# Kernel optimization log

Hardware: AMD Instinct MI355X
Metric: run time of the kernel (lower is better)

## Reference

```python
import jax, jax.numpy as jnp
import numpy as np

# Model dims
B, S, H = 1, 1024, 2048
NH, NKV, DH = 32, 8, 64
G = NH // NKV            # GQA group size
E, K, I = 8, 2, 2048     # experts, top_k, intermediate
ALPHA, LIMIT = 1.702, 7.0
EPS = 1e-5
SCALE = DH ** -0.5


def rmsnorm(x, g):
    return x * jax.lax.rsqrt(jnp.mean(x * x, axis=-1, keepdims=True) + EPS) * g


def setup_inputs() -> dict:
    key = jax.random.key(0)
    ks = jax.random.split(key, 24)
    w = lambda k, shp: jax.random.normal(k, shp, dtype=jnp.float32) * 0.02
    causal = jnp.where(jnp.tril(jnp.ones((S, S), dtype=bool)), 0.0, -1e9).astype(jnp.float32)
    return {
        "hidden_states": jax.random.normal(ks[0], (B, S, H), dtype=jnp.float32),
        "attention_bias": causal[None, None, :, :],           # [1,1,S,S]
        "ln1_g": jnp.ones((H,), jnp.float32),
        "ln2_g": jnp.ones((H,), jnp.float32),
        "Wq": w(ks[1], (NH * DH, H)),  "bq": w(ks[2], (NH * DH,)),
        "Wk": w(ks[3], (NKV * DH, H)), "bk": w(ks[4], (NKV * DH,)),
        "Wv": w(ks[5], (NKV * DH, H)), "bv": w(ks[6], (NKV * DH,)),
        "Wo": w(ks[7], (H, NH * DH)),  "bo": w(ks[8], (H,)),
        "sinks": w(ks[9], (NH,)),
        "router_w": w(ks[10], (E, H)), "router_b": w(ks[11], (E,)),
        "We_gate": w(ks[12], (E, I, H)), "be_gate": w(ks[13], (E, I)),
        "We_up":   w(ks[14], (E, I, H)), "be_up":   w(ks[15], (E, I)),
        "We_down": w(ks[16], (E, H, I)), "be_down": w(ks[17], (E, H)),
    }


def reference(hidden_states, attention_bias, ln1_g, ln2_g,
              Wq, bq, Wk, bk, Wv, bv, Wo, bo, sinks,
              router_w, router_b,
              We_gate, be_gate, We_up, be_up, We_down, be_down):
    x = hidden_states
    # ---- pre-norm sink attention ----
    xn = rmsnorm(x, ln1_g)
    q = (xn @ Wq.T + bq).reshape(B, S, NH, DH).transpose(0, 2, 1, 3)    # [B,NH,S,DH]
    k = (xn @ Wk.T + bk).reshape(B, S, NKV, DH).transpose(0, 2, 1, 3)   # [B,NKV,S,DH]
    v = (xn @ Wv.T + bv).reshape(B, S, NKV, DH).transpose(0, 2, 1, 3)
    # GQA: replicate each kv head G times consecutively (repeat_kv)
    k = jnp.repeat(k, G, axis=1)
    v = jnp.repeat(v, G, axis=1)
    scores = jnp.einsum('bhqd,bhkd->bhqk', q, k) * SCALE + attention_bias  # [B,NH,S,S]
    sink_col = jnp.broadcast_to(sinks.reshape(1, NH, 1, 1), (B, NH, S, 1))
    combined = jnp.concatenate([scores, sink_col], axis=-1)               # [B,NH,S,S+1]
    probs = jax.nn.softmax(combined, axis=-1)[..., :-1]                   # drop sink
    attn = jnp.einsum('bhqk,bhkd->bhqd', probs, v)
    attn = attn.transpose(0, 2, 1, 3).reshape(B, S, NH * DH)
    h = x + (attn @ Wo.T + bo)
    # ---- pre-norm MoE FFN ----
    hn = rmsnorm(h, ln2_g)
    router_logits = hn @ router_w.T + router_b                            # [B,S,E]
    rw, sel = jax.lax.top_k(router_logits, K)
    rw = jax.nn.softmax(rw, axis=-1)                                      # [B,S,K]
    # dense per-expert MLP over all tokens (matches the exported loop)
    gate = jnp.einsum('bsh,eih->bsei', hn, We_gate) + be_gate             # [B,S,E,I]
    up = jnp.einsum('bsh,eih->bsei', hn, We_up) + be_up
    gate_c = jnp.minimum(gate, LIMIT)
    up_c = jnp.clip(up, -LIMIT, LIMIT)
    glu = gate_c * jax.nn.sigmoid(ALPHA * gate_c)
    gated = (up_c + 1.0) * glu
    down = jnp.einsum('bsei,ehi->bseh', gated, We_down) + be_down         # [B,S,E,H]
    # per-token expert weight: sum_k rw * (sel == e)
    wts = jnp.sum(rw[..., None] * (sel[..., None] == jnp.arange(E)), axis=2)  # [B,S,E]
    moe = jnp.einsum('bseh,bse->bsh', down, wts)
    return h + moe
```

## Files before the change

### kernel.cpp

```cpp
#include <hip/hip_runtime.h>
#include <hip/hip_bf16.h>

#define HD 2048
#define SEQ 1024
#define NHEAD 32
#define NKVH 8
#define DHEAD 64
#define NEXP 8
#define INTER 2048
#define SCALE 0.125f
#define ALPHA 1.702f
#define LIMIT 7.0f

typedef __attribute__((ext_vector_type(8))) short short8;
typedef __attribute__((ext_vector_type(4))) short short4v;
typedef __attribute__((ext_vector_type(4))) float f32x4;

__device__ __forceinline__ unsigned short f2bf(float f) {
  union { float f; unsigned u; } v; v.f = f;
  unsigned r = v.u + 0x7fffu + ((v.u >> 16) & 1u);
  return (unsigned short)(r >> 16);
}
__device__ __forceinline__ float bf2f(unsigned short h) {
  union { unsigned u; float f; } v; v.u = ((unsigned)h) << 16; return v.f;
}
__device__ __forceinline__ void split2(float f, unsigned short& hi, unsigned short& lo) {
  hi = f2bf(f);
  lo = f2bf(f - bf2f(hi));
}

__device__ __forceinline__ f32x4 mfma32(short8 a, short8 b, f32x4 c) {
  return __builtin_amdgcn_mfma_f32_16x16x32_bf16(a, b, c, 0, 0, 0);
}

__device__ __forceinline__ void gl_lds16(const float* g, float* l) {
  __builtin_amdgcn_global_load_lds(
      (const __attribute__((address_space(1))) unsigned int*)g,
      (__attribute__((address_space(3))) unsigned int*)l, 16, 0, 0);
}

__global__ __launch_bounds__(256) void rmsnorm_split_kernel(
    const float* __restrict__ x, const float* __restrict__ gamma,
    unsigned short* __restrict__ oh, unsigned short* __restrict__ ol) {
  int row = blockIdx.x, tid = threadIdx.x;
  const float* xr = x + (size_t)row * HD;
  float v[8];
#pragma unroll
  for (int i = 0; i < 8; ++i) v[i] = xr[tid * 8 + i];
  float ss = 0.f;
#pragma unroll
  for (int i = 0; i < 8; ++i) ss += v[i] * v[i];
#pragma unroll
  for (int off = 32; off; off >>= 1) ss += __shfl_xor(ss, off, 64);
  __shared__ float wss[4];
  if ((tid & 63) == 0) wss[tid >> 6] = ss;
  __syncthreads();
  float rs = rsqrtf((wss[0] + wss[1] + wss[2] + wss[3]) * (1.0f / HD) + 1e-5f);
  short8 vh, vl;
#pragma unroll
  for (int i = 0; i < 8; ++i) {
    float val = v[i] * rs * gamma[tid * 8 + i];
    unsigned short h, lo;
    split2(val, h, lo);
    vh[i] = (short)h;
    vl[i] = (short)lo;
  }
  *(short8*)(oh + (size_t)row * HD + tid * 8) = vh;
  *(short8*)(ol + (size_t)row * HD + tid * 8) = vl;
}

__global__ __launch_bounds__(256) void rmsnorm_plain_kernel(
    const float* __restrict__ x, const float* __restrict__ gamma,
    unsigned short* __restrict__ out) {
  int row = blockIdx.x, tid = threadIdx.x;
  const float* xr = x + (size_t)row * HD;
  float v[8];
#pragma unroll
  for (int i = 0; i < 8; ++i) v[i] = xr[tid * 8 + i];
  float ss = 0.f;
#pragma unroll
  for (int i = 0; i < 8; ++i) ss += v[i] * v[i];
#pragma unroll
  for (int off = 32; off; off >>= 1) ss += __shfl_xor(ss, off, 64);
  __shared__ float wss[4];
  if ((tid & 63) == 0) wss[tid >> 6] = ss;
  __syncthreads();
  float rs = rsqrtf((wss[0] + wss[1] + wss[2] + wss[3]) * (1.0f / HD) + 1e-5f);
  short8 o;
#pragma unroll
  for (int i = 0; i < 8; ++i) o[i] = (short)f2bf(v[i] * rs * gamma[tid * 8 + i]);
  *(short8*)(out + (size_t)row * HD + tid * 8) = o;
}

template <int MT, int NS, bool SPLIT, int EPI>
__global__ __launch_bounds__(256) void gemm_gl(
    const unsigned short* __restrict__ Ah, const unsigned short* __restrict__ Al,
    int ldA,
    const float* __restrict__ W0, const float* __restrict__ W1,
    const float* __restrict__ W2,
    const float* __restrict__ b0, const float* __restrict__ b1,
    const float* __restrict__ b2,
    const float* __restrict__ resid,
    const int* __restrict__ counts, const int* __restrict__ arows,
    const int* __restrict__ orows,
    unsigned short* __restrict__ oh0, unsigned short* __restrict__ ol0,
    unsigned short* __restrict__ oh1, unsigned short* __restrict__ ol1,
    unsigned short* __restrict__ oh2, unsigned short* __restrict__ ol2,
    float* __restrict__ f0, unsigned short* __restrict__ gated,
    int M, int Kd) {
  constexpr int NR = NS * 16;
  constexpr int NMAT = (EPI == 4) ? 2 : 1;
  constexpr int NI = NMAT * NR / 16;
  __shared__ __align__(16) float lw[2][NMAT][NR][64];
  int tid = threadIdx.x, l = tid & 63, w = tid >> 6;
  int g = l >> 4, q = l & 15;
  int n0 = blockIdx.x * NR;

  const float* WbM[NMAT];
  const float* bias;
  const float* bias2 = nullptr;
  int nloc = n0, e = 0;
  if constexpr (EPI == 0) {
    if (n0 < NHEAD * DHEAD) {
      WbM[0] = W0; bias = b0;
    } else if (n0 < NHEAD * DHEAD + NKVH * DHEAD) {
      WbM[0] = W1; bias = b1; nloc = n0 - NHEAD * DHEAD;
    } else {
      WbM[0] = W2; bias = b2; nloc = n0 - (NHEAD * DHEAD + NKVH * DHEAD);
    }
  } else if constexpr (EPI == 1) {
    WbM[0] = W0; bias = b0;
  } else if constexpr (EPI == 3) {
    e = blockIdx.z;
    WbM[0] = W0 + (size_t)e * HD * INTER;
    bias = b0 + (size_t)e * HD;
  } else {
    e = blockIdx.z;
    WbM[0] = W0 + (size_t)e * INTER * HD;
    WbM[1] = W1 + (size_t)e * INTER * HD;
    bias = b0 + (size_t)e * INTER;
    bias2 = b1 + (size_t)e * INTER;
  }
  int cnt = (EPI >= 3) ? counts[e] : M;

  const float* sptr[NI];
  float* sdst0[NI];
  float* sdst1[NI];
#pragma unroll
  for (int j = 0; j < NI; ++j) {
    int gi = w * NI + j;
    int mat = gi / (NR / 4);
    int rr = (gi % (NR / 4)) * 4;
    int r = rr + (l >> 4);
    int gs = ((l & 15) ^ (r & 7)) * 4;
    sptr[j] = WbM[mat] + (size_t)(nloc + r) * Kd + gs;
    sdst0[j] = &lw[0][mat][rr][0];
    sdst1[j] = &lw[1][mat][rr][0];
  }
  auto stage = [&](int buf, int kc) {
#pragma unroll
    for (int j = 0; j < NI; ++j)
      gl_lds16(sptr[j] + kc, buf ? sdst1[j] : sdst0[j]);
  };

  int mstart = (EPI <= 1) ? blockIdx.y : 0;
  int mstep = (EPI <= 1) ? gridDim.y : 1;
  constexpr int MG = MT * 64;

  for (int mg = mstart; mg * MG < cnt; mg += mstep) {
    int mb = mg * MG + w * (MT * 16);
    const unsigned short* ap[MT];
    const unsigned short* apl[MT];
#pragma unroll
    for (int mt = 0; mt < MT; ++mt) {
      int mm = min(mb + mt * 16 + q, cnt - 1);
      int ar = (EPI >= 3) ? arows[e * SEQ + mm] : mm;
      ap[mt] = Ah + (size_t)ar * ldA + 8 * g;
      if constexpr (SPLIT) apl[mt] = Al + (size_t)ar * ldA + 8 * g;
    }
    f32x4 acc[NMAT][MT][NS];
#pragma unroll
    for (int m2 = 0; m2 < NMAT; ++m2)
#pragma unroll
      for (int mt = 0; mt < MT; ++mt)
#pragma unroll
        for (int ns = 0; ns < NS; ++ns)
          acc[m2][mt][ns] = (f32x4){0.f, 0.f, 0.f, 0.f};

    stage(0, 0);
    short8 ab[2][MT], abl[2][MT];
#pragma unroll
    for (int mt = 0; mt < MT; ++mt) {
      ab[0][mt] = *(const short8*)(ap[mt]);
      ab[1][mt] = *(const short8*)(ap[mt] + 32);
      if constexpr (SPLIT) {
        abl[0][mt] = *(const short8*)(apl[mt]);
        abl[1][mt] = *(const short8*)(apl[mt] + 32);
      }
    }
    __syncthreads();

    int nc = Kd / 64;
    for (int c = 0; c < nc; ++c) {
      int u = c & 1;
      if (c + 1 < nc) stage(u ^ 1, (c + 1) * 64);
#pragma unroll
      for (int kh = 0; kh < 2; ++kh) {
        short8 acur[MT], acl[MT];
#pragma unroll
        for (int mt = 0; mt < MT; ++mt) {
          acur[mt] = ab[kh][mt];
          if constexpr (SPLIT) acl[mt] = abl[kh][mt];
        }
        int kn = c * 64 + kh * 32 + 64;
        if (kn < Kd) {
#pragma unroll
          for (int mt = 0; mt < MT; ++mt) {
            ab[kh][mt] = *(const short8*)(ap[mt] + kn);
            if constexpr (SPLIT) abl[kh][mt] = *(const short8*)(apl[mt] + kn);
          }
        }
        short8 wh[NMAT][NS], wl[NMAT][NS];
#pragma unroll
        for (int m2 = 0; m2 < NMAT; ++m2)
#pragma unroll
          for (int ns = 0; ns < NS; ++ns) {
            int row = ns * 16 + q;
            int r7 = q & 7;
            int i0 = ((kh * 8 + g * 2) ^ r7) * 16;
            int i1 = ((kh * 8 + g * 2 + 1) ^ r7) * 16;
            const char* base = (const char*)&lw[u][m2][row][0];
            float4 v0 = *(const float4*)(base + i0);
            float4 v1 = *(const float4*)(base + i1);
            float vv[8] = {v0.x, v0.y, v0.z, v0.w, v1.x, v1.y, v1.z, v1.w};
#pragma unroll
            for (int jj = 0; jj < 8; ++jj) {
              if constexpr (SPLIT) {
                unsigned short h, lo;
                split2(vv[jj], h, lo);
                wh[m2][ns][jj] = (short)h;
                wl[m2][ns][jj] = (short)lo;
              } else {
                wh[m2][ns][jj] = (short)f2bf(vv[jj]);
              }
            }
          }
#pragma unroll
        for (int m2 = 0; m2 < NMAT; ++m2)
#pragma unroll
          for (int mt = 0; mt < MT; ++mt)
#pragma unroll
            for (int ns = 0; ns < NS; ++ns) {
              acc[m2][mt][ns] = mfma32(acur[mt], wh[m2][ns], acc[m2][mt][ns]);
              if constexpr (SPLIT) {
                acc[m2][mt][ns] = mfma32(acur[mt], wl[m2][ns], acc[m2][mt][ns]);
                acc[m2][mt][ns] = mfma32(acl[mt], wh[m2][ns], acc[m2][mt][ns]);
              }
            }
      }
      __syncthreads();
    }
#pragma unroll
    for (int ns = 0; ns < NS; ++ns) {
      int ncol = nloc + ns * 16 + q;
      float bs = bias[ncol];
      float bs2 = (EPI == 4) ? bias2[ncol] : 0.f;
#pragma unroll
      for (int mt = 0; mt < MT; ++mt) {
#pragma unroll
        for (int r = 0; r < 4; ++r) {
          int mr = mb + mt * 16 + 4 * g + r;
          float val = acc[0][mt][ns][r] + bs;
          if constexpr (EPI == 0) {
            unsigned short h, lo;
            split2(val, h, lo);
            if (n0 < NHEAD * DHEAD) {
              oh0[(size_t)mr * (NHEAD * DHEAD) + ncol] = h;
              ol0[(size_t)mr * (NHEAD * DHEAD) + ncol] = lo;
            } else if (n0 < NHEAD * DHEAD + NKVH * DHEAD) {
              oh1[(size_t)mr * (NKVH * DHEAD) + ncol] = h;
              ol1[(size_t)mr * (NKVH * DHEAD) + ncol] = lo;
            } else {
              oh2[(size_t)ncol * SEQ + mr] = h;
              ol2[(size_t)ncol * SEQ + mr] = lo;
            }
          } else if constexpr (EPI == 1) {
            f0[(size_t)mr * HD + ncol] = val + resid[(size_t)mr * HD + ncol];
          } else if constexpr (EPI == 3) {
            if (mr < cnt) {
              int slot = orows[e * SEQ + mr];
              f0[(size_t)slot * HD + ncol] = val;
            }
          } else {
            if (mr < cnt) {
              int slot = orows[e * SEQ + mr];
              float up = acc[1][mt][ns][r] + bs2;
              float gc = fminf(val, LIMIT);
              float uc = fminf(fmaxf(up, -LIMIT), LIMIT);
              float glu = gc / (1.f + __expf(-ALPHA * gc));
              gated[(size_t)slot * INTER + ncol] = f2bf((uc + 1.f) * glu);
            }
          }
        }
      }
    }
  }
}

__global__ __launch_bounds__(256) void attn_kernel(
    const unsigned short* __restrict__ Qh, const unsigned short* __restrict__ Ql,
    const unsigned short* __restrict__ Kh, const unsigned short* __restrict__ Kl,
    const unsigned short* __restrict__ Vh, const unsigned short* __restrict__ Vl,
    const float* __restrict__ sinks, unsigned short* __restrict__ outh,
    unsigned short* __restrict__ outl) {
  __shared__ __align__(16) unsigned short pbuf[4][2][16][40];
  int l = threadIdx.x & 63, widx = threadIdx.x >> 6;
  int wid = blockIdx.x * 4 + widx;
  int head = wid >> 6, qt = wid & 63;
  int q0 = qt * 16;
  int g = l >> 4, q = l & 15;
  int kvh = head >> 2;
  size_t qoff = (size_t)(q0 + q) * (NHEAD * DHEAD) + head * DHEAD + 8 * g;
  short8 qh0 = *(const short8*)(Qh + qoff);
  short8 qh1 = *(const short8*)(Qh + qoff + 32);
  short8 ql0 = *(const short8*)(Ql + qoff);
  short8 ql1 = *(const short8*)(Ql + qoff + 32);
  float m = sinks[head];
  float lsum = 1.0f;
  f32x4 o[4] = {{0, 0, 0, 0}, {0, 0, 0, 0}, {0, 0, 0, 0}, {0, 0, 0, 0}};
  int qglob = q0 + q;
  for (int kt = 0; kt <= qt; kt += 2) {
    bool hasB = (kt + 1) <= qt;
    size_t koff = (size_t)(kt * 16 + q) * (NKVH * DHEAD) + kvh * DHEAD + 8 * g;
    f32x4 stA = {0, 0, 0, 0};
    {
      short8 kh0 = *(const short8*)(Kh + koff);
      short8 kh1 = *(const short8*)(Kh + koff + 32);
      short8 kl0 = *(const short8*)(Kl + koff);
      short8 kl1 = *(const short8*)(Kl + koff + 32);
      stA = mfma32(kh0, qh0, stA);
      stA = mfma32(kh0, ql0, stA);
      stA = mfma32(kl0, qh0, stA);
      stA = mfma32(kh1, qh1, stA);
      stA = mfma32(kh1, ql1, stA);
      stA = mfma32(kl1, qh1, stA);
    }
    f32x4 stB = {0, 0, 0, 0};
    if (hasB) {
      size_t koff2 = koff + (size_t)16 * (NKVH * DHEAD);
      short8 kh0 = *(const short8*)(Kh + koff2);
      short8 kh1 = *(const short8*)(Kh + koff2 + 32);
      short8 kl0 = *(const short8*)(Kl + koff2);
      short8 kl1 = *(const short8*)(Kl + koff2 + 32);
      stB = mfma32(kh0, qh0, stB);
      stB = mfma32(kh0, ql0, stB);
      stB = mfma32(kl0, qh0, stB);
      stB = mfma32(kh1, qh1, stB);
      stB = mfma32(kh1, ql1, stB);
      stB = mfma32(kl1, qh1, stB);
    }
    float sA[4], sB[4];
#pragma unroll
    for (int r = 0; r < 4; ++r) {
      int keyA = kt * 16 + 4 * g + r;
      sA[r] = (keyA <= qglob) ? stA[r] * SCALE : -1e30f;
      sB[r] = (hasB && keyA + 16 <= qglob) ? stB[r] * SCALE : -1e30f;
    }
    float mt = fmaxf(fmaxf(fmaxf(sA[0], sA[1]), fmaxf(sA[2], sA[3])),
                     fmaxf(fmaxf(sB[0], sB[1]), fmaxf(sB[2], sB[3])));
    mt = fmaxf(mt, __shfl_xor(mt, 16, 64));
    mt = fmaxf(mt, __shfl_xor(mt, 32, 64));
    float mnew = fmaxf(m, mt);
    float corr = __expf(m - mnew);
    float pA[4], pB[4];
    float rsum = 0.f;
#pragma unroll
    for (int r = 0; r < 4; ++r) {
      pA[r] = __expf(sA[r] - mnew);
      pB[r] = __expf(sB[r] - mnew);
      rsum += pA[r] + pB[r];
    }
    rsum += __shfl_xor(rsum, 16, 64);
    rsum += __shfl_xor(rsum, 32, 64);
    lsum = lsum * corr + rsum;
    m = mnew;
#pragma unroll
    for (int dt = 0; dt < 4; ++dt)
#pragma unroll
      for (int r = 0; r < 4; ++r) o[dt][r] *= corr;
    unsigned short ph[8], pl[8];
#pragma unroll
    for (int r = 0; r < 4; ++r) {
      split2(pA[r], ph[r], pl[r]);
      split2(pB[r], ph[4 + r], pl[4 + r]);
    }
    short4v wAh = {(short)ph[0], (short)ph[1], (short)ph[2], (short)ph[3]};
    short4v wBh = {(short)ph[4], (short)ph[5], (short)ph[6], (short)ph[7]};
    short4v wAl = {(short)pl[0], (short)pl[1], (short)pl[2], (short)pl[3]};
    short4v wBl = {(short)pl[4], (short)pl[5], (short)pl[6], (short)pl[7]};
    *(short4v*)&pbuf[widx][0][q][4 * g] = wAh;
    *(short4v*)&pbuf[widx][0][q][16 + 4 * g] = wBh;
    *(short4v*)&pbuf[widx][1][q][4 * g] = wAl;
    *(short4v*)&pbuf[widx][1][q][16 + 4 * g] = wBl;
    asm volatile("s_waitcnt lgkmcnt(0)" ::: "memory");
    short8 pbh = *(const short8*)&pbuf[widx][0][q][8 * g];
    short8 pbl = *(const short8*)&pbuf[widx][1][q][8 * g];
    size_t vbase = (size_t)(kvh * DHEAD) * SEQ + kt * 16 + 8 * g;
#pragma unroll
    for (int dt = 0; dt < 4; ++dt) {
      size_t voff = vbase + (size_t)(dt * 16 + q) * SEQ;
      short8 vh8 = *(const short8*)(Vh + voff);
      short8 vl8 = *(const short8*)(Vl + voff);
      o[dt] = mfma32(vh8, pbh, o[dt]);
      o[dt] = mfma32(vh8, pbl, o[dt]);
      o[dt] = mfma32(vl8, pbh, o[dt]);
    }
  }
  float inv = 1.0f / lsum;
#pragma unroll
  for (int dt = 0; dt < 4; ++dt)
#pragma unroll
    for (int r = 0; r < 4; ++r) {
      float val = o[dt][r] * inv;
      unsigned short h, lo;
      split2(val, h, lo);
      size_t idx = (size_t)qglob * (NHEAD * DHEAD) + head * DHEAD + dt * 16 + 4 * g + r;
      outh[idx] = h;
      outl[idx] = lo;
    }
}

__global__ __launch_bounds__(64) void router_kernel(
    const float* __restrict__ h, const float* __restrict__ gamma,
    const float* __restrict__ rw, const float* __restrict__ rb,
    float* __restrict__ wsel, int* __restrict__ counts,
    int* __restrict__ lists, int* __restrict__ slotof) {
  int t = blockIdx.x;
  int l = threadIdx.x;
  const float* hr = h + (size_t)t * HD;
  double ss = 0.0;
  for (int i = l; i < HD; i += 64) {
    double x = (double)hr[i];
    ss += x * x;
  }
#pragma unroll
  for (int off = 32; off; off >>= 1) ss += __shfl_xor(ss, off, 64);
  double rs = rsqrt(ss * (1.0 / HD) + 1e-5);
  double acc[NEXP];
#pragma unroll
  for (int e = 0; e < NEXP; ++e) acc[e] = 0.0;
  for (int i = l; i < HD; i += 64) {
    double xh = (double)hr[i] * rs * (double)gamma[i];
#pragma unroll
    for (int e = 0; e < NEXP; ++e) acc[e] += xh * (double)rw[e * HD + i];
  }
#pragma unroll
  for (int e = 0; e < NEXP; ++e)
#pragma unroll
    for (int off = 32; off; off >>= 1) acc[e] += __shfl_xor(acc[e], off, 64);
  if (l == 0) {
    double lg[NEXP];
#pragma unroll
    for (int e = 0; e < NEXP; ++e) lg[e] = acc[e] + (double)rb[e];
    int e0 = 0;
#pragma unroll
    for (int e = 1; e < NEXP; ++e)
      if (lg[e] > lg[e0]) e0 = e;
    int e1 = -1;
#pragma unroll
    for (int e = 0; e < NEXP; ++e)
      if (e != e0 && (e1 < 0 || lg[e] > lg[e1])) e1 = e;
    double d = exp(lg[e1] - lg[e0]);
    float p0 = (float)(1.0 / (1.0 + d)), p1 = (float)(d / (1.0 + d));
    wsel[2 * t] = p0;
    wsel[2 * t + 1] = p1;
    int s0 = atomicAdd(&counts[e0], 1);
    lists[e0 * SEQ + s0] = t;
    slotof[e0 * SEQ + s0] = 2 * t;
    int s1 = atomicAdd(&counts[e1], 1);
    lists[e1 * SEQ + s1] = t;
    slotof[e1 * SEQ + s1] = 2 * t + 1;
  }
}

__global__ __launch_bounds__(256) void reduce_kernel(
    const float* __restrict__ hbuf, const float* __restrict__ scr,
    const float* __restrict__ wsel, float* __restrict__ out) {
  int t = blockIdx.x;
  int c = threadIdx.x * 8;
  float w0 = wsel[2 * t], w1 = wsel[2 * t + 1];
  size_t hb = (size_t)t * HD + c;
  size_t s0 = (size_t)(2 * t) * HD + c;
  size_t s1 = (size_t)(2 * t + 1) * HD + c;
#pragma unroll
  for (int j = 0; j < 2; ++j) {
    float4 hv = *(const float4*)(hbuf + hb + 4 * j);
    float4 a = *(const float4*)(scr + s0 + 4 * j);
    float4 b = *(const float4*)(scr + s1 + 4 * j);
    float4 r;
    r.x = hv.x + w0 * a.x + w1 * b.x;
    r.y = hv.y + w0 * a.y + w1 * b.y;
    r.z = hv.z + w0 * a.z + w1 * b.z;
    r.w = hv.w + w0 * a.w + w1 * b.w;
    *(float4*)(out + hb + 4 * j) = r;
  }
}

extern "C" void kernel_launch(void* const* d_in, const int* in_sizes, int n_in,
                              void* d_out, int out_size, void* d_ws,
                              size_t ws_size, hipStream_t stream) {
  const float* x = (const float*)d_in[0];
  const float* ln1 = (const float*)d_in[2];
  const float* ln2 = (const float*)d_in[3];
  const float* Wq = (const float*)d_in[4];
  const float* bq = (const float*)d_in[5];
  const float* Wk = (const float*)d_in[6];
  const float* bk = (const float*)d_in[7];
  const float* Wv = (const float*)d_in[8];
  const float* bv = (const float*)d_in[9];
  const float* Wo = (const float*)d_in[10];
  const float* bo = (const float*)d_in[11];
  const float* sinks = (const float*)d_in[12];
  const float* rw = (const float*)d_in[13];
  const float* rb = (const float*)d_in[14];
  const float* Wg = (const float*)d_in[15];
  const float* bg = (const float*)d_in[16];
  const float* Wu = (const float*)d_in[17];
  const float* bu = (const float*)d_in[18];
  const float* Wd = (const float*)d_in[19];
  const float* bd = (const float*)d_in[20];
  float* out = (float*)d_out;

  char* ws = (char*)d_ws;
  size_t off = 0;
  auto alloc = [&](size_t bytes) {
    void* p = ws + off;
    off += (bytes + 255) & ~(size_t)255;
    return p;
  };
  unsigned short* xnh = (unsigned short*)alloc((size_t)SEQ * HD * 2);
  unsigned short* xnl = (unsigned short*)alloc((size_t)SEQ * HD * 2);
  unsigned short* qbh = (unsigned short*)alloc((size_t)SEQ * NHEAD * DHEAD * 2);
  unsigned short* qbl = (unsigned short*)alloc((size_t)SEQ * NHEAD * DHEAD * 2);
  unsigned short* kbh = (unsigned short*)alloc((size_t)SEQ * NKVH * DHEAD * 2);
  unsigned short* kbl = (unsigned short*)alloc((size_t)SEQ * NKVH * DHEAD * 2);
  unsigned short* vth = (unsigned short*)alloc((size_t)NKVH * DHEAD * SEQ * 2);
  unsigned short* vtl = (unsigned short*)alloc((size_t)NKVH * DHEAD * SEQ * 2);
  unsigned short* ath = (unsigned short*)alloc((size_t)SEQ * NHEAD * DHEAD * 2);
  unsigned short* atl = (unsigned short*)alloc((size_t)SEQ * NHEAD * DHEAD * 2);
  float* hbuf = (float*)alloc((size_t)SEQ * HD * 4);
  unsigned short* hn = (unsigned short*)alloc((size_t)SEQ * HD * 2);
  float* wsel = (float*)alloc((size_t)SEQ * 2 * 4);
  int* counts = (int*)alloc(NEXP * 4);
  int* lists = (int*)alloc((size_t)NEXP * SEQ * 4);
  int* slotof = (int*)alloc((size_t)NEXP * SEQ * 4);
  unsigned short* gated = (unsigned short*)alloc((size_t)2 * SEQ * INTER * 2);
  float* scr = (float*)alloc((size_t)2 * SEQ * HD * 4);
  (void)ws_size;
  (void)off;

  rmsnorm_split_kernel<<<SEQ, 256, 0, stream>>>(x, ln1, xnh, xnl);
  gemm_gl<2, 2, true, 0><<<dim3(96, 8, 1), 256, 0, stream>>>(
      xnh, xnl, HD, Wq, Wk, Wv, bq, bk, bv, nullptr, nullptr, nullptr, nullptr,
      qbh, qbl, kbh, kbl, vth, vtl, nullptr, nullptr, SEQ, HD);
  attn_kernel<<<NHEAD * 64 / 4, 256, 0, stream>>>(qbh, qbl, kbh, kbl, vth, vtl,
                                                  sinks, ath, atl);
  gemm_gl<2, 2, true, 1><<<dim3(64, 8, 1), 256, 0, stream>>>(
      ath, atl, NHEAD * DHEAD, Wo, nullptr, nullptr, bo, nullptr, nullptr, x,
      nullptr, nullptr, nullptr, nullptr, nullptr, nullptr, nullptr, nullptr,
      nullptr, hbuf, nullptr, SEQ, NHEAD * DHEAD);
  rmsnorm_plain_kernel<<<SEQ, 256, 0, stream>>>(hbuf, ln2, hn);
  hipMemsetAsync(counts, 0, NEXP * sizeof(int), stream);
  router_kernel<<<SEQ, 64, 0, stream>>>(hbuf, ln2, rw, rb, wsel, counts, lists,
                                        slotof);
  gemm_gl<5, 2, false, 4><<<dim3(64, 1, 8), 256, 0, stream>>>(
      hn, nullptr, HD, Wg, Wu, nullptr, bg, bu, nullptr, nullptr, counts, lists,
      slotof, nullptr, nullptr, nullptr, nullptr, nullptr, nullptr, nullptr,
      gated, SEQ, HD);
  gemm_gl<5, 2, false, 3><<<dim3(64, 1, 8), 256, 0, stream>>>(
      gated, nullptr, INTER, Wd, nullptr, nullptr, bd, nullptr, nullptr,
      nullptr, counts, slotof, slotof, nullptr, nullptr, nullptr, nullptr,
      nullptr, nullptr, scr, nullptr, SEQ, INTER);
  reduce_kernel<<<SEQ, 256, 0, stream>>>(hbuf, scr, wsel, out);
}
```

Baseline: 563.9 us.

## Split-K the MoE expert GEMMs with atomic accumulation and separate activation kernel

Adds a K-split template parameter so the gate/up and down expert GEMMs run with two K-slices per tile, doubling grid blocks (64x2x8) and accumulating partial sums into zeroed fp32 buffers via atomicAdd. The gate/up epilogue now writes raw fp32 gate and up values, and a new act_kernel applies the clamp/sigmoid GLU and converts to bf16. This targets underfilled grids (512 blocks on a 256-CU device) and the serial K loop per block. In exchange it adds memsets, fp32 atomics, and extra global traffic for raw buffers (2x16MB written and read), plus one more launch.

```diff
diff --git a/kernel.cpp b/kernel.cpp
--- a/kernel.cpp
+++ b/kernel.cpp
@@ -92,7 +92,7 @@
   *(short8*)(out + (size_t)row * HD + tid * 8) = o;
 }
 
-template <int MT, int NS, bool SPLIT, int EPI>
+template <int MT, int NS, bool SPLIT, int EPI, int KSP>
 __global__ __launch_bounds__(256) void gemm_gl(
     const unsigned short* __restrict__ Ah, const unsigned short* __restrict__ Al,
     int ldA,
@@ -106,7 +106,7 @@
     unsigned short* __restrict__ oh0, unsigned short* __restrict__ ol0,
     unsigned short* __restrict__ oh1, unsigned short* __restrict__ ol1,
     unsigned short* __restrict__ oh2, unsigned short* __restrict__ ol2,
-    float* __restrict__ f0, unsigned short* __restrict__ gated,
+    float* __restrict__ f0, float* __restrict__ f1,
     int M, int Kd) {
   constexpr int NR = NS * 16;
   constexpr int NMAT = (EPI == 4) ? 2 : 1;
@@ -143,6 +143,18 @@
   }
   int cnt = (EPI >= 3) ? counts[e] : M;
 
+  int kstart = 0, kLen = Kd;
+  int mstart = 0, mstep = 1;
+  bool kfirst = true;
+  if constexpr (EPI <= 1) {
+    mstart = blockIdx.y;
+    mstep = gridDim.y;
+  } else {
+    kLen = Kd / KSP;
+    kstart = blockIdx.y * kLen;
+    kfirst = (blockIdx.y == 0);
+  }
+
   const float* sptr[NI];
   float* sdst0[NI];
   float* sdst1[NI];
@@ -153,7 +165,7 @@
     int rr = (gi % (NR / 4)) * 4;
     int r = rr + (l >> 4);
     int gs = ((l & 15) ^ (r & 7)) * 4;
-    sptr[j] = WbM[mat] + (size_t)(nloc + r) * Kd + gs;
+    sptr[j] = WbM[mat] + (size_t)(nloc + r) * Kd + kstart + gs;
     sdst0[j] = &lw[0][mat][rr][0];
     sdst1[j] = &lw[1][mat][rr][0];
   }
@@ -163,8 +175,6 @@
       gl_lds16(sptr[j] + kc, buf ? sdst1[j] : sdst0[j]);
   };
 
-  int mstart = (EPI <= 1) ? blockIdx.y : 0;
-  int mstep = (EPI <= 1) ? gridDim.y : 1;
   constexpr int MG = MT * 64;
 
   for (int mg = mstart; mg * MG < cnt; mg += mstep) {
@@ -175,8 +185,8 @@
     for (int mt = 0; mt < MT; ++mt) {
       int mm = min(mb + mt * 16 + q, cnt - 1);
       int ar = (EPI >= 3) ? arows[e * SEQ + mm] : mm;
-      ap[mt] = Ah + (size_t)ar * ldA + 8 * g;
-      if constexpr (SPLIT) apl[mt] = Al + (size_t)ar * ldA + 8 * g;
+      ap[mt] = Ah + (size_t)ar * ldA + kstart + 8 * g;
+      if constexpr (SPLIT) apl[mt] = Al + (size_t)ar * ldA + kstart + 8 * g;
     }
     f32x4 acc[NMAT][MT][NS];
 #pragma unroll
@@ -200,7 +210,7 @@
     }
     __syncthreads();
 
-    int nc = Kd / 64;
+    int nc = kLen / 64;
     for (int c = 0; c < nc; ++c) {
       int u = c & 1;
       if (c + 1 < nc) stage(u ^ 1, (c + 1) * 64);
@@ -213,7 +223,7 @@
           if constexpr (SPLIT) acl[mt] = abl[kh][mt];
         }
         int kn = c * 64 + kh * 32 + 64;
-        if (kn < Kd) {
+        if (kn < kLen) {
 #pragma unroll
           for (int mt = 0; mt < MT; ++mt) {
             ab[kh][mt] = *(const short8*)(ap[mt] + kn);
@@ -263,8 +273,9 @@
 #pragma unroll
     for (int ns = 0; ns < NS; ++ns) {
       int ncol = nloc + ns * 16 + q;
-      float bs = bias[ncol];
-      float bs2 = (EPI == 4) ? bias2[ncol] : 0.f;
+      float bs = (EPI >= 3 && !kfirst) ? 0.f : bias[ncol];
+      float bs2 = 0.f;
+      if constexpr (EPI == 4) bs2 = kfirst ? bias2[ncol] : 0.f;
 #pragma unroll
       for (int mt = 0; mt < MT; ++mt) {
 #pragma unroll
@@ -289,22 +300,50 @@
           } else if constexpr (EPI == 3) {
             if (mr < cnt) {
               int slot = orows[e * SEQ + mr];
-              f0[(size_t)slot * HD + ncol] = val;
+              if constexpr (KSP == 1) {
+                f0[(size_t)slot * HD + ncol] = val;
+              } else {
+                atomicAdd(&f0[(size_t)slot * HD + ncol], val);
+              }
             }
           } else {
             if (mr < cnt) {
               int slot = orows[e * SEQ + mr];
               float up = acc[1][mt][ns][r] + bs2;
-              float gc = fminf(val, LIMIT);
-              float uc = fminf(fmaxf(up, -LIMIT), LIMIT);
-              float glu = gc / (1.f + __expf(-ALPHA * gc));
-              gated[(size_t)slot * INTER + ncol] = f2bf((uc + 1.f) * glu);
+              if constexpr (KSP == 1) {
+                f0[(size_t)slot * INTER + ncol] = val;
+                f1[(size_t)slot * INTER + ncol] = up;
+              } else {
+                atomicAdd(&f0[(size_t)slot * INTER + ncol], val);
+                atomicAdd(&f1[(size_t)slot * INTER + ncol], up);
+              }
             }
           }
         }
       }
     }
   }
+}
+
+__global__ __launch_bounds__(256) void act_kernel(
+    const float* __restrict__ rg, const float* __restrict__ ru,
+    unsigned short* __restrict__ gated) {
+  size_t base = (size_t)blockIdx.x * INTER + threadIdx.x * 8;
+  float4 g0 = *(const float4*)(rg + base);
+  float4 g1 = *(const float4*)(rg + base + 4);
+  float4 u0 = *(const float4*)(ru + base);
+  float4 u1 = *(const float4*)(ru + base + 4);
+  float gv[8] = {g0.x, g0.y, g0.z, g0.w, g1.x, g1.y, g1.z, g1.w};
+  float uv[8] = {u0.x, u0.y, u0.z, u0.w, u1.x, u1.y, u1.z, u1.w};
+  short8 o;
+#pragma unroll
+  for (int j = 0; j < 8; ++j) {
+    float gc = fminf(gv[j], LIMIT);
+    float uc = fminf(fmaxf(uv[j], -LIMIT), LIMIT);
+    float glu = gc / (1.f + __expf(-ALPHA * gc));
+    o[j] = (short)f2bf((uc + 1.f) * glu);
+  }
+  *(short8*)(gated + base) = o;
 }
 
 __global__ __launch_bounds__(256) void attn_kernel(
@@ -554,18 +593,20 @@
   int* counts = (int*)alloc(NEXP * 4);
   int* lists = (int*)alloc((size_t)NEXP * SEQ * 4);
   int* slotof = (int*)alloc((size_t)NEXP * SEQ * 4);
+  float* rawg = (float*)alloc((size_t)2 * SEQ * INTER * 4);
+  float* rawu = (float*)alloc((size_t)2 * SEQ * INTER * 4);
   unsigned short* gated = (unsigned short*)alloc((size_t)2 * SEQ * INTER * 2);
   float* scr = (float*)alloc((size_t)2 * SEQ * HD * 4);
   (void)ws_size;
   (void)off;
 
   rmsnorm_split_kernel<<<SEQ, 256, 0, stream>>>(x, ln1, xnh, xnl);
-  gemm_gl<2, 2, true, 0><<<dim3(96, 8, 1), 256, 0, stream>>>(
+  gemm_gl<2, 2, true, 0, 1><<<dim3(96, 8, 1), 256, 0, stream>>>(
       xnh, xnl, HD, Wq, Wk, Wv, bq, bk, bv, nullptr, nullptr, nullptr, nullptr,
       qbh, qbl, kbh, kbl, vth, vtl, nullptr, nullptr, SEQ, HD);
   attn_kernel<<<NHEAD * 64 / 4, 256, 0, stream>>>(qbh, qbl, kbh, kbl, vth, vtl,
                                                   sinks, ath, atl);
-  gemm_gl<2, 2, true, 1><<<dim3(64, 8, 1), 256, 0, stream>>>(
+  gemm_gl<2, 2, true, 1, 1><<<dim3(64, 8, 1), 256, 0, stream>>>(
       ath, atl, NHEAD * DHEAD, Wo, nullptr, nullptr, bo, nullptr, nullptr, x,
       nullptr, nullptr, nullptr, nullptr, nullptr, nullptr, nullptr, nullptr,
       nullptr, hbuf, nullptr, SEQ, NHEAD * DHEAD);
@@ -573,11 +614,15 @@
   hipMemsetAsync(counts, 0, NEXP * sizeof(int), stream);
   router_kernel<<<SEQ, 64, 0, stream>>>(hbuf, ln2, rw, rb, wsel, counts, lists,
                                         slotof);
-  gemm_gl<5, 2, false, 4><<<dim3(64, 1, 8), 256, 0, stream>>>(
+  hipMemsetAsync(rawg, 0, (size_t)2 * SEQ * INTER * 4, stream);
+  hipMemsetAsync(rawu, 0, (size_t)2 * SEQ * INTER * 4, stream);
+  gemm_gl<5, 2, false, 4, 2><<<dim3(64, 2, 8), 256, 0, stream>>>(
       hn, nullptr, HD, Wg, Wu, nullptr, bg, bu, nullptr, nullptr, counts, lists,
-      slotof, nullptr, nullptr, nullptr, nullptr, nullptr, nullptr, nullptr,
-      gated, SEQ, HD);
-  gemm_gl<5, 2, false, 3><<<dim3(64, 1, 8), 256, 0, stream>>>(
+      slotof, nullptr, nullptr, nullptr, nullptr, nullptr, nullptr, rawg, rawu,
+      SEQ, HD);
+  act_kernel<<<2 * SEQ, 256, 0, stream>>>(rawg, rawu, gated);
+  hipMemsetAsync(scr, 0, (size_t)2 * SEQ * HD * 4, stream);
+  gemm_gl<5, 2, false, 3, 2><<<dim3(64, 2, 8), 256, 0, stream>>>(
       gated, nullptr, INTER, Wd, nullptr, nullptr, bd, nullptr, nullptr,
       nullptr, counts, slotof, slotof, nullptr, nullptr, nullptr, nullptr,
       nullptr, nullptr, scr, nullptr, SEQ, INTER);
```

New measurement: 651.2 us. +15.5%, slower.
